# Kernel tuning notes

Measured on AMD Instinct MI355X. Metric: run time of the kernel, lower is better.

## Reference

```python
import jax, jax.numpy as jnp
import numpy as np

SOFTMAX_SCALE = 0.5  # passed as scalar arg in the original op

def setup_inputs() -> dict:
    key = jax.random.key(0)
    ks = jax.random.split(key, 6)
    B, Sq, H, D, Smax = 8, 1, 32, 128, 4096
    q = jax.random.normal(ks[0], (B, Sq, H, D), dtype=jnp.float32)
    k = jax.random.normal(ks[1], (B, Sq, H, D), dtype=jnp.float32)
    v = jax.random.normal(ks[2], (B, Sq, H, D), dtype=jnp.float32)
    kcache = jax.random.normal(ks[3], (B, Smax, H, D), dtype=jnp.float32)
    vcache = jax.random.normal(ks[4], (B, Smax, H, D), dtype=jnp.float32)
    # current cache occupancy per batch; ensure seqlen + Sq <= Smax
    seqlen = jax.random.randint(ks[5], (B,), 0, Smax - Sq).astype(jnp.int32)
    return {"q": q, "k": k, "v": v, "kcache": kcache, "vcache": vcache, "seqlen": seqlen}

def reference(q, k, v, kcache, vcache, seqlen):
    # Semantics of flash_attn_with_kvcache: append k/v into the cache at
    # offset seqlen[b], then causally attend q over cache[: seqlen[b] + S_new].
    # Causal alignment is bottom-right: query i maps to key position
    # seqlen + S_new - S_q + i.
    B, Sq, H, D = q.shape
    Smax = kcache.shape[1]
    Snew = k.shape[1]
    pos_k = jnp.arange(Smax)          # [Smax]
    pos_q = jnp.arange(Sq)            # [Sq]

    def one_batch(qb, kb, vb, kcb, vcb, sl):
        # qb: [Sq,H,D]; kcb/vcb: [Smax,H,D]; sl: scalar int32
        kc = jax.lax.dynamic_update_slice(kcb, kb, (sl, 0, 0))
        vc = jax.lax.dynamic_update_slice(vcb, vb, (sl, 0, 0))
        scores = jnp.einsum('qhd,khd->hqk', qb, kc) * SOFTMAX_SCALE  # [H,Sq,Smax]
        kmax = sl + Snew - Sq + pos_q                                # [Sq]
        mask = pos_k[None, :] <= kmax[:, None]                       # [Sq,Smax]
        scores = jnp.where(mask[None, :, :], scores, -jnp.inf)
        p = jax.nn.softmax(scores, axis=-1)
        return jnp.einsum('hqk,khd->qhd', p, vc)                     # [Sq,H,D]

    return jax.vmap(one_batch)(q, k, v, kcache, vcache, seqlen)
```

## Files before the change

kernel.cpp:

```cpp
#include <hip/hip_runtime.h>
#include <math.h>

#define B_    8
#define H_    32
#define D_    128
#define SMAX_ 4096
#define HD_   (H_ * D_)
#define SCALE 0.5f
#define PSTRIDE (D_ + 2)

__global__ __launch_bounds__(512, 4)
void attn_partial(const float* __restrict__ q,
                  const float* __restrict__ knew,
                  const float* __restrict__ vnew,
                  const float* __restrict__ kcache,
                  const float* __restrict__ vcache,
                  const int* __restrict__ seqlen,
                  float* __restrict__ ws,
                  int nsplit)
{
    const int blk   = blockIdx.x;
    const int b     = blk & (B_ - 1);
    const int split = blk / B_;
    const int t     = threadIdx.x;
    const int h     = t >> 4;
    const int ds    = (t & 15) * 8;
    const int sl    = seqlen[b];

    float* wsp = ws + (((size_t)b * nsplit + split) * H_ + h) * PSTRIDE;

    float qf[8];
    {
        const float* qp = q + (b * H_ + h) * D_ + ds;
        float4 t0 = *(const float4*)(qp);
        float4 t1 = *(const float4*)(qp + 4);
        qf[0]=t0.x; qf[1]=t0.y; qf[2]=t0.z; qf[3]=t0.w;
        qf[4]=t1.x; qf[5]=t1.y; qf[6]=t1.z; qf[7]=t1.w;
    }

    float m = -1e30f, l = 0.f;
    float acc[8];
    #pragma unroll
    for (int j = 0; j < 8; ++j) acc[j] = 0.f;

    const size_t pstep = (size_t)HD_ * nsplit;
    const float* kb = kcache + (size_t)b * SMAX_ * HD_ + t * 8;
    const float* vb = vcache + (size_t)b * SMAX_ * HD_ + t * 8;

#define STEP1(KP, VP) do {                                                    \
    float4 k0 = *(const float4*)(KP);                                         \
    float4 k1 = *(const float4*)((KP)+4);                                     \
    float4 v0 = *(const float4*)(VP);                                         \
    float4 v1 = *(const float4*)((VP)+4);                                     \
    float s = qf[0]*k0.x+qf[1]*k0.y+qf[2]*k0.z+qf[3]*k0.w                     \
            + qf[4]*k1.x+qf[5]*k1.y+qf[6]*k1.z+qf[7]*k1.w;                    \
    s += __shfl_xor(s, 1); s += __shfl_xor(s, 2);                             \
    s += __shfl_xor(s, 4); s += __shfl_xor(s, 8);                             \
    s *= SCALE;                                                               \
    float mn = fmaxf(m, s);                                                   \
    float sc = __expf(m - mn);                                                \
    float pr = __expf(s - mn);                                                \
    m = mn; l = l * sc + pr;                                                  \
    acc[0]=fmaf(pr,v0.x,acc[0]*sc); acc[1]=fmaf(pr,v0.y,acc[1]*sc);           \
    acc[2]=fmaf(pr,v0.z,acc[2]*sc); acc[3]=fmaf(pr,v0.w,acc[3]*sc);           \
    acc[4]=fmaf(pr,v1.x,acc[4]*sc); acc[5]=fmaf(pr,v1.y,acc[5]*sc);           \
    acc[6]=fmaf(pr,v1.z,acc[6]*sc); acc[7]=fmaf(pr,v1.w,acc[7]*sc);           \
} while (0)

    int p = split;
    const float* kp = kb + (size_t)split * HD_;
    const float* vp = vb + (size_t)split * HD_;
    for (; p + nsplit < sl; p += 2 * nsplit) {
        const float* kq = kp + pstep;
        const float* vq = vp + pstep;
        float4 a0 = *(const float4*)(kp);
        float4 a1 = *(const float4*)(kp + 4);
        float4 b0 = *(const float4*)(kq);
        float4 b1 = *(const float4*)(kq + 4);
        float4 u0 = *(const float4*)(vp);
        float4 u1 = *(const float4*)(vp + 4);
        float4 w0 = *(const float4*)(vq);
        float4 w1 = *(const float4*)(vq + 4);

        float s0 = qf[0]*a0.x+qf[1]*a0.y+qf[2]*a0.z+qf[3]*a0.w
                 + qf[4]*a1.x+qf[5]*a1.y+qf[6]*a1.z+qf[7]*a1.w;
        float s1 = qf[0]*b0.x+qf[1]*b0.y+qf[2]*b0.z+qf[3]*b0.w
                 + qf[4]*b1.x+qf[5]*b1.y+qf[6]*b1.z+qf[7]*b1.w;
        s0 += __shfl_xor(s0, 1); s0 += __shfl_xor(s0, 2);
        s0 += __shfl_xor(s0, 4); s0 += __shfl_xor(s0, 8);
        s1 += __shfl_xor(s1, 1); s1 += __shfl_xor(s1, 2);
        s1 += __shfl_xor(s1, 4); s1 += __shfl_xor(s1, 8);
        s0 *= SCALE; s1 *= SCALE;

        float mn  = fmaxf(m, fmaxf(s0, s1));
        float sc  = __expf(m - mn);
        float pr0 = __expf(s0 - mn);
        float pr1 = __expf(s1 - mn);
        m = mn;
        l = l * sc + pr0 + pr1;
        acc[0] = fmaf(pr1,w0.x, fmaf(pr0,u0.x, acc[0]*sc));
        acc[1] = fmaf(pr1,w0.y, fmaf(pr0,u0.y, acc[1]*sc));
        acc[2] = fmaf(pr1,w0.z, fmaf(pr0,u0.z, acc[2]*sc));
        acc[3] = fmaf(pr1,w0.w, fmaf(pr0,u0.w, acc[3]*sc));
        acc[4] = fmaf(pr1,w1.x, fmaf(pr0,u1.x, acc[4]*sc));
        acc[5] = fmaf(pr1,w1.y, fmaf(pr0,u1.y, acc[5]*sc));
        acc[6] = fmaf(pr1,w1.z, fmaf(pr0,u1.z, acc[6]*sc));
        acc[7] = fmaf(pr1,w1.w, fmaf(pr0,u1.w, acc[7]*sc));
        kp += 2 * pstep;
        vp += 2 * pstep;
    }
    if (p < sl) {
        STEP1(kp, vp);
    }
    if ((sl & (nsplit - 1)) == split) {
        const float* kn = knew + (size_t)b * HD_ + t * 8;
        const float* vn = vnew + (size_t)b * HD_ + t * 8;
        STEP1(kn, vn);
    }
#undef STEP1

    if ((t & 15) == 0) { wsp[0] = m; wsp[1] = l; }
    float* op = wsp + 2 + ds;
    *(float4*)(op)     = make_float4(acc[0], acc[1], acc[2], acc[3]);
    *(float4*)(op + 4) = make_float4(acc[4], acc[5], acc[6], acc[7]);
}

__global__ __launch_bounds__(128)
void attn_combine(const float* __restrict__ ws, float* __restrict__ out, int nsplit)
{
    const int bh = blockIdx.x;
    const int b  = bh >> 5;
    const int h  = bh & (H_ - 1);
    const int t  = threadIdx.x;

    __shared__ float sm_e[512];
    __shared__ float sm_w[2];

    const size_t sstride = (size_t)H_ * PSTRIDE;
    const float* base = ws + ((size_t)b * nsplit * H_ + h) * PSTRIDE;

    float mx = -1e30f;
    for (int s = t; s < nsplit; s += 128) mx = fmaxf(mx, base[(size_t)s * sstride]);
    #pragma unroll
    for (int off = 1; off < 64; off <<= 1) mx = fmaxf(mx, __shfl_xor(mx, off));
    if ((t & 63) == 0) sm_w[t >> 6] = mx;
    __syncthreads();
    const float mt = fmaxf(sm_w[0], sm_w[1]);
    __syncthreads();

    float le = 0.f;
    for (int s = t; s < nsplit; s += 128) {
        const float* p = base + (size_t)s * sstride;
        float ms = p[0], ls = p[1];
        float e = (ls > 0.f) ? __expf(ms - mt) : 0.f;
        sm_e[s] = e;
        le += ls * e;
    }
    #pragma unroll
    for (int off = 1; off < 64; off <<= 1) le += __shfl_xor(le, off);
    if ((t & 63) == 0) sm_w[t >> 6] = le;
    __syncthreads();
    const float lt = sm_w[0] + sm_w[1];

    const float* ab = base + 2 + t;
    float a = 0.f;
    #pragma unroll 8
    for (int s = 0; s < nsplit; ++s) {
        a += sm_e[s] * ab[(size_t)s * sstride];
    }
    out[bh * D_ + t] = a / lt;
}

extern "C" void kernel_launch(void* const* d_in, const int* in_sizes, int n_in,
                              void* d_out, int out_size, void* d_ws, size_t ws_size,
                              hipStream_t stream) {
    const float* q  = (const float*)d_in[0];
    const float* k  = (const float*)d_in[1];
    const float* v  = (const float*)d_in[2];
    const float* kc = (const float*)d_in[3];
    const float* vc = (const float*)d_in[4];
    const int*   sl = (const int*)d_in[5];
    float* out = (float*)d_out;
    float* ws  = (float*)d_ws;

    int nsplit = 128;
    while (nsplit > 1 &&
           (size_t)B_ * nsplit * H_ * PSTRIDE * sizeof(float) > ws_size) {
        nsplit >>= 1;
    }

    attn_partial<<<B_ * nsplit, 512, 0, stream>>>(q, k, v, kc, vc, sl, ws, nsplit);
    attn_combine<<<B_ * H_, 128, 0, stream>>>(ws, out, nsplit);
}
```

Measured before the change: 151.5 us.

## Split heads across four block groups with float4 per thread for more parallelism

The partial-attention kernel now launches four times as many blocks. Each block covers 8 heads with 256 threads, and each thread handles 4 dims instead of 8, so a head's dot product is reduced over a 32-lane shuffle. The workspace layout moves m and l to the end of a padded 132-float stride, and the split count is fixed at 128 with no check against workspace size. The aim is more waves in flight and better latency hiding for the memory-bound cache stream. The cost is an extra shuffle step per key and four times the per-block overhead, including the repeated seqlen load.

```diff
diff --git a/kernel.cpp b/kernel.cpp
--- a/kernel.cpp
+++ b/kernel.cpp
@@ -1,95 +1,78 @@
 #include <hip/hip_runtime.h>
 #include <math.h>
 
-#define B_    8
-#define H_    32
-#define D_    128
-#define SMAX_ 4096
-#define HD_   (H_ * D_)
-#define SCALE 0.5f
-#define PSTRIDE (D_ + 2)
+#define B_     8
+#define H_     32
+#define D_     128
+#define SMAX_  4096
+#define HD_    (H_ * D_)
+#define SCALE  0.5f
+#define PSPLIT 128
+#define NHG    4
+#define PSTRIDE 132
 
-__global__ __launch_bounds__(512, 4)
+__global__ __launch_bounds__(256, 8)
 void attn_partial(const float* __restrict__ q,
                   const float* __restrict__ knew,
                   const float* __restrict__ vnew,
                   const float* __restrict__ kcache,
                   const float* __restrict__ vcache,
                   const int* __restrict__ seqlen,
-                  float* __restrict__ ws,
-                  int nsplit)
+                  float* __restrict__ ws)
 {
     const int blk   = blockIdx.x;
     const int b     = blk & (B_ - 1);
-    const int split = blk / B_;
+    const int split = (blk >> 3) & (PSPLIT - 1);
+    const int hg    = blk >> 10;
     const int t     = threadIdx.x;
-    const int h     = t >> 4;
-    const int ds    = (t & 15) * 8;
-    const int sl    = seqlen[b];
+    const int h     = hg * 8 + (t >> 5);
+    const int dl    = t & 31;
+    const int ds    = dl * 4;
 
-    float* wsp = ws + (((size_t)b * nsplit + split) * H_ + h) * PSTRIDE;
+    const int sl = seqlen[b];
 
-    float qf[8];
-    {
-        const float* qp = q + (b * H_ + h) * D_ + ds;
-        float4 t0 = *(const float4*)(qp);
-        float4 t1 = *(const float4*)(qp + 4);
-        qf[0]=t0.x; qf[1]=t0.y; qf[2]=t0.z; qf[3]=t0.w;
-        qf[4]=t1.x; qf[5]=t1.y; qf[6]=t1.z; qf[7]=t1.w;
-    }
+    const float4 qf = *(const float4*)(q + ((b * H_ + h) * D_ + ds));
 
     float m = -1e30f, l = 0.f;
-    float acc[8];
-    #pragma unroll
-    for (int j = 0; j < 8; ++j) acc[j] = 0.f;
+    float4 acc = make_float4(0.f, 0.f, 0.f, 0.f);
 
-    const size_t pstep = (size_t)HD_ * nsplit;
-    const float* kb = kcache + (size_t)b * SMAX_ * HD_ + t * 8;
-    const float* vb = vcache + (size_t)b * SMAX_ * HD_ + t * 8;
+    const size_t poff  = (size_t)hg * 1024 + (size_t)t * 4;
+    const float* kb = kcache + (size_t)b * SMAX_ * HD_ + poff;
+    const float* vb = vcache + (size_t)b * SMAX_ * HD_ + poff;
+    const size_t pstep = (size_t)HD_ * PSPLIT;
 
 #define STEP1(KP, VP) do {                                                    \
     float4 k0 = *(const float4*)(KP);                                         \
-    float4 k1 = *(const float4*)((KP)+4);                                     \
     float4 v0 = *(const float4*)(VP);                                         \
-    float4 v1 = *(const float4*)((VP)+4);                                     \
-    float s = qf[0]*k0.x+qf[1]*k0.y+qf[2]*k0.z+qf[3]*k0.w                     \
-            + qf[4]*k1.x+qf[5]*k1.y+qf[6]*k1.z+qf[7]*k1.w;                    \
-    s += __shfl_xor(s, 1); s += __shfl_xor(s, 2);                             \
-    s += __shfl_xor(s, 4); s += __shfl_xor(s, 8);                             \
+    float s = qf.x*k0.x + qf.y*k0.y + qf.z*k0.z + qf.w*k0.w;                  \
+    s += __shfl_xor(s, 1);  s += __shfl_xor(s, 2);  s += __shfl_xor(s, 4);    \
+    s += __shfl_xor(s, 8);  s += __shfl_xor(s, 16);                           \
     s *= SCALE;                                                               \
     float mn = fmaxf(m, s);                                                   \
     float sc = __expf(m - mn);                                                \
     float pr = __expf(s - mn);                                                \
     m = mn; l = l * sc + pr;                                                  \
-    acc[0]=fmaf(pr,v0.x,acc[0]*sc); acc[1]=fmaf(pr,v0.y,acc[1]*sc);           \
-    acc[2]=fmaf(pr,v0.z,acc[2]*sc); acc[3]=fmaf(pr,v0.w,acc[3]*sc);           \
-    acc[4]=fmaf(pr,v1.x,acc[4]*sc); acc[5]=fmaf(pr,v1.y,acc[5]*sc);           \
-    acc[6]=fmaf(pr,v1.z,acc[6]*sc); acc[7]=fmaf(pr,v1.w,acc[7]*sc);           \
+    acc.x = fmaf(pr, v0.x, acc.x * sc);                                       \
+    acc.y = fmaf(pr, v0.y, acc.y * sc);                                       \
+    acc.z = fmaf(pr, v0.z, acc.z * sc);                                       \
+    acc.w = fmaf(pr, v0.w, acc.w * sc);                                       \
 } while (0)
 
     int p = split;
     const float* kp = kb + (size_t)split * HD_;
     const float* vp = vb + (size_t)split * HD_;
-    for (; p + nsplit < sl; p += 2 * nsplit) {
-        const float* kq = kp + pstep;
-        const float* vq = vp + pstep;
+    for (; p + PSPLIT < sl; p += 2 * PSPLIT) {
         float4 a0 = *(const float4*)(kp);
-        float4 a1 = *(const float4*)(kp + 4);
-        float4 b0 = *(const float4*)(kq);
-        float4 b1 = *(const float4*)(kq + 4);
+        float4 b0 = *(const float4*)(kp + pstep);
         float4 u0 = *(const float4*)(vp);
-        float4 u1 = *(const float4*)(vp + 4);
-        float4 w0 = *(const float4*)(vq);
-        float4 w1 = *(const float4*)(vq + 4);
+        float4 w0 = *(const float4*)(vp + pstep);
 
-        float s0 = qf[0]*a0.x+qf[1]*a0.y+qf[2]*a0.z+qf[3]*a0.w
-                 + qf[4]*a1.x+qf[5]*a1.y+qf[6]*a1.z+qf[7]*a1.w;
-        float s1 = qf[0]*b0.x+qf[1]*b0.y+qf[2]*b0.z+qf[3]*b0.w
-                 + qf[4]*b1.x+qf[5]*b1.y+qf[6]*b1.z+qf[7]*b1.w;
-        s0 += __shfl_xor(s0, 1); s0 += __shfl_xor(s0, 2);
-        s0 += __shfl_xor(s0, 4); s0 += __shfl_xor(s0, 8);
-        s1 += __shfl_xor(s1, 1); s1 += __shfl_xor(s1, 2);
-        s1 += __shfl_xor(s1, 4); s1 += __shfl_xor(s1, 8);
+        float s0 = qf.x*a0.x + qf.y*a0.y + qf.z*a0.z + qf.w*a0.w;
+        float s1 = qf.x*b0.x + qf.y*b0.y + qf.z*b0.z + qf.w*b0.w;
+        s0 += __shfl_xor(s0, 1);  s0 += __shfl_xor(s0, 2);  s0 += __shfl_xor(s0, 4);
+        s0 += __shfl_xor(s0, 8);  s0 += __shfl_xor(s0, 16);
+        s1 += __shfl_xor(s1, 1);  s1 += __shfl_xor(s1, 2);  s1 += __shfl_xor(s1, 4);
+        s1 += __shfl_xor(s1, 8);  s1 += __shfl_xor(s1, 16);
         s0 *= SCALE; s1 *= SCALE;
 
         float mn  = fmaxf(m, fmaxf(s0, s1));
@@ -98,49 +81,44 @@
         float pr1 = __expf(s1 - mn);
         m = mn;
         l = l * sc + pr0 + pr1;
-        acc[0] = fmaf(pr1,w0.x, fmaf(pr0,u0.x, acc[0]*sc));
-        acc[1] = fmaf(pr1,w0.y, fmaf(pr0,u0.y, acc[1]*sc));
-        acc[2] = fmaf(pr1,w0.z, fmaf(pr0,u0.z, acc[2]*sc));
-        acc[3] = fmaf(pr1,w0.w, fmaf(pr0,u0.w, acc[3]*sc));
-        acc[4] = fmaf(pr1,w1.x, fmaf(pr0,u1.x, acc[4]*sc));
-        acc[5] = fmaf(pr1,w1.y, fmaf(pr0,u1.y, acc[5]*sc));
-        acc[6] = fmaf(pr1,w1.z, fmaf(pr0,u1.z, acc[6]*sc));
-        acc[7] = fmaf(pr1,w1.w, fmaf(pr0,u1.w, acc[7]*sc));
+        acc.x = fmaf(pr1, w0.x, fmaf(pr0, u0.x, acc.x * sc));
+        acc.y = fmaf(pr1, w0.y, fmaf(pr0, u0.y, acc.y * sc));
+        acc.z = fmaf(pr1, w0.z, fmaf(pr0, u0.z, acc.z * sc));
+        acc.w = fmaf(pr1, w0.w, fmaf(pr0, u0.w, acc.w * sc));
         kp += 2 * pstep;
         vp += 2 * pstep;
     }
     if (p < sl) {
         STEP1(kp, vp);
     }
-    if ((sl & (nsplit - 1)) == split) {
-        const float* kn = knew + (size_t)b * HD_ + t * 8;
-        const float* vn = vnew + (size_t)b * HD_ + t * 8;
+    if ((sl & (PSPLIT - 1)) == split) {
+        const float* kn = knew + (size_t)b * HD_ + poff;
+        const float* vn = vnew + (size_t)b * HD_ + poff;
         STEP1(kn, vn);
     }
 #undef STEP1
 
-    if ((t & 15) == 0) { wsp[0] = m; wsp[1] = l; }
-    float* op = wsp + 2 + ds;
-    *(float4*)(op)     = make_float4(acc[0], acc[1], acc[2], acc[3]);
-    *(float4*)(op + 4) = make_float4(acc[4], acc[5], acc[6], acc[7]);
+    float* wsp = ws + (((size_t)b * PSPLIT + split) * H_ + h) * PSTRIDE;
+    *(float4*)(wsp + ds) = acc;
+    if (dl == 0) { wsp[128] = m; wsp[129] = l; }
 }
 
 __global__ __launch_bounds__(128)
-void attn_combine(const float* __restrict__ ws, float* __restrict__ out, int nsplit)
+void attn_combine(const float* __restrict__ ws, float* __restrict__ out)
 {
     const int bh = blockIdx.x;
     const int b  = bh >> 5;
     const int h  = bh & (H_ - 1);
     const int t  = threadIdx.x;
 
-    __shared__ float sm_e[512];
+    __shared__ float sm_e[PSPLIT];
     __shared__ float sm_w[2];
 
     const size_t sstride = (size_t)H_ * PSTRIDE;
-    const float* base = ws + ((size_t)b * nsplit * H_ + h) * PSTRIDE;
+    const float* base = ws + ((size_t)b * PSPLIT * H_ + h) * PSTRIDE;
 
     float mx = -1e30f;
-    for (int s = t; s < nsplit; s += 128) mx = fmaxf(mx, base[(size_t)s * sstride]);
+    for (int s = t; s < PSPLIT; s += 128) mx = fmaxf(mx, base[(size_t)s * sstride + 128]);
     #pragma unroll
     for (int off = 1; off < 64; off <<= 1) mx = fmaxf(mx, __shfl_xor(mx, off));
     if ((t & 63) == 0) sm_w[t >> 6] = mx;
@@ -149,9 +127,9 @@
     __syncthreads();
 
     float le = 0.f;
-    for (int s = t; s < nsplit; s += 128) {
+    for (int s = t; s < PSPLIT; s += 128) {
         const float* p = base + (size_t)s * sstride;
-        float ms = p[0], ls = p[1];
+        float ms = p[128], ls = p[129];
         float e = (ls > 0.f) ? __expf(ms - mt) : 0.f;
         sm_e[s] = e;
         le += ls * e;
@@ -162,10 +140,10 @@
     __syncthreads();
     const float lt = sm_w[0] + sm_w[1];
 
-    const float* ab = base + 2 + t;
+    const float* ab = base + t;
     float a = 0.f;
     #pragma unroll 8
-    for (int s = 0; s < nsplit; ++s) {
+    for (int s = 0; s < PSPLIT; ++s) {
         a += sm_e[s] * ab[(size_t)s * sstride];
     }
     out[bh * D_ + t] = a / lt;
@@ -183,12 +161,6 @@
     float* out = (float*)d_out;
     float* ws  = (float*)d_ws;
 
-    int nsplit = 128;
-    while (nsplit > 1 &&
-           (size_t)B_ * nsplit * H_ * PSTRIDE * sizeof(float) > ws_size) {
-        nsplit >>= 1;
-    }
-
-    attn_partial<<<B_ * nsplit, 512, 0, stream>>>(q, k, v, kc, vc, sl, ws, nsplit);
-    attn_combine<<<B_ * H_, 128, 0, stream>>>(ws, out, nsplit);
+    attn_partial<<<NHG * PSPLIT * B_, 256, 0, stream>>>(q, k, v, kc, vc, sl, ws);
+    attn_combine<<<B_ * H_, 128, 0, stream>>>(ws, out);
 }
```

After: 158.1 us. +4.3%, slower.
